# Kernel tuning notes

Hardware: AMD Instinct MI355X
Metric: run time of the kernel (lower is better)

Reference implementation:

```python
import jax, jax.numpy as jnp
import numpy as np

B, GS, IN, HID = 256, 32, 512, 1024
HW = GS * GS

def setup_inputs() -> dict:
    key = jax.random.key(0)
    ks = jax.random.split(key, 18)
    s = 0.02
    return {
        "grid": jax.random.normal(ks[0], (B, 1, GS, GS), jnp.float32),
        "conv1_w": jax.random.normal(ks[1], (8, 1, 3, 3), jnp.float32) * s,
        "conv1_b": jax.random.normal(ks[2], (8,), jnp.float32) * s,
        "conv2_w": jax.random.normal(ks[3], (16, 8, 3, 3), jnp.float32) * s,
        "conv2_b": jax.random.normal(ks[4], (16,), jnp.float32) * s,
        "lin_w": jax.random.normal(ks[5], (IN, HW * 16), jnp.float32) * s,
        "lin_b": jax.random.normal(ks[6], (IN,), jnp.float32) * s,
        "gru_wih": jax.random.normal(ks[7], (3 * HID, IN + HW + 1), jnp.float32) * s,
        "gru_whh": jax.random.normal(ks[8], (3 * HID, HID), jnp.float32) * s,
        "gru_bih": jax.random.normal(ks[9], (3 * HID,), jnp.float32) * s,
        "gru_bhh": jax.random.normal(ks[10], (3 * HID,), jnp.float32) * s,
        "write_w": jax.random.normal(ks[11], (HW, HID), jnp.float32) * s,
        "write_b": jax.random.normal(ks[12], (HW,), jnp.float32) * s,
        "inc_w": jax.random.normal(ks[13], (1, HID), jnp.float32) * s,
        "inc_b": jax.random.normal(ks[14], (1,), jnp.float32) * s,
        "term_w": jax.random.normal(ks[15], (1, HID), jnp.float32) * s,
        "term_b": jax.random.normal(ks[16], (1,), jnp.float32) * s,
        "max_steps": 100,
    }

def _conv(x, w, b):
    y = jax.lax.conv_general_dilated(x, w, (1, 1), "SAME",
                                     dimension_numbers=("NCHW", "OIHW", "NCHW"))
    return y + b[None, :, None, None]

def _gru_cell(x, h, wih, whh, bih, bhh):
    gi = x @ wih.T + bih            # (B, 3H)
    gh = h @ whh.T + bhh
    ir, iz, inn = jnp.split(gi, 3, axis=1)
    hr, hz, hn = jnp.split(gh, 3, axis=1)
    r = jax.nn.sigmoid(ir + hr)
    z = jax.nn.sigmoid(iz + hz)
    n = jnp.tanh(inn + r * hn)
    return (1.0 - z) * n + z * h

def reference(grid, conv1_w, conv1_b, conv2_w, conv2_b, lin_w, lin_b,
              gru_wih, gru_whh, gru_bih, gru_bhh,
              write_w, write_b, inc_w, inc_b, term_w, term_b, max_steps):
    bsz = grid.shape[0]
    feat = jax.nn.relu(_conv(grid, conv1_w, conv1_b))
    feat = jax.nn.relu(_conv(feat, conv2_w, conv2_b))
    feat = feat.reshape(bsz, -1) @ lin_w.T + lin_b     # (B, IN), torch Flatten is channel-major

    def step(carry, _):
        h, mask, count, done = carry
        x = jnp.concatenate([feat, mask, count], axis=1)
        h2 = _gru_cell(x, h, gru_wih, gru_whh, gru_bih, gru_bhh)
        write = jax.nn.sigmoid(h2 @ write_w.T + write_b)
        inc = jax.nn.sigmoid(h2 @ inc_w.T + inc_b)
        term = jax.nn.sigmoid(h2 @ term_w.T + term_b)
        upd = jnp.logical_not(done)
        h_n = jnp.where(upd, h2, h)
        mask_n = jnp.where(upd, mask + write, mask)
        count_n = jnp.where(upd, count + inc, count)
        done_n = jnp.logical_or(done, jnp.all(term > 0.5))
        return (h_n, mask_n, count_n, done_n), None

    init = (jnp.zeros((bsz, HID), grid.dtype),
            jnp.zeros((bsz, HW), grid.dtype),
            jnp.zeros((bsz, 1), grid.dtype),
            jnp.array(False))
    (h, mask, count, done), _ = jax.lax.scan(step, init, None, length=max_steps)
    return count, mask
```

## Files before the change

### kernel.cpp

```cpp
#include <hip/hip_runtime.h>
#include <hip/hip_cooperative_groups.h>

namespace cg = cooperative_groups;

#define DEVI static __device__ __forceinline__

typedef __attribute__((ext_vector_type(8))) short s8v;
typedef __attribute__((ext_vector_type(4))) float f32x4;
typedef unsigned short us_t;
typedef unsigned int u32;

constexpr int NT_ = 256;
constexpr int B_ = 256, HW_ = 1024, IN_ = 512, HID_ = 1024, H3_ = 3072;
constexpr int XD_ = 1537;
constexpr int FLAT_ = 16384;

constexpr int OFF_WIHFBF = 0;
constexpr int OFF_WIHM2  = 393216;
constexpr int OFF_WHHBF  = 3538944;
constexpr int OFF_WIHC   = 5111808;
constexpr int OFF_CNTD   = 5114880;
constexpr int OFF_FLAGS  = 5115136;
constexpr int OFF_FEATBF = 5115264;
constexpr int OFF_GI     = 5180800;
constexpr int OFF_GH     = 5967232;
constexpr int OFF_H0     = 6753664;
constexpr int OFF_H1     = 7015808;
constexpr int OFF_WSIG   = 7277952;
constexpr int OFF_HHI    = 7540096;
constexpr int OFF_WSIG2  = 7671168;
constexpr int OFF_C2BF   = 7933312;
constexpr int OFF_LINWBF = 10030464;
constexpr int OFF_PART = OFF_GI;
constexpr int OFF_PW   = OFF_C2BF;
constexpr int OFF_WWBF = 10292608;
constexpr int OFF_PA2  = 14224768;

struct Params {
  const float* grid;
  const float* c1w; const float* c1b;
  const float* c2w; const float* c2b;
  const float* linw; const float* linb;
  const float* wih; const float* whh;
  const float* bih; const float* bhh;
  const float* ww;  const float* wb;
  const float* incw; const float* incb;
  const float* termw; const float* termb;
  const int* max_steps;
  float* out;
  float* ws;
};

DEVI float sigm(float x) { return 1.f / (1.f + __expf(-x)); }
DEVI float tanh_(float x) { return 1.f - 2.f / (__expf(2.f * x) + 1.f); }
DEVI float2 ld2(const float* p) { return *(const float2*)p; }
DEVI void ld4(float* d, const float* p) {
  float4 v = *(const float4*)p; d[0] = v.x; d[1] = v.y; d[2] = v.z; d[3] = v.w;
}
DEVI us_t f2bf(float x) {
  union { float f; u32 u; } v; v.f = x;
  u32 r = v.u + 0x7FFFu + ((v.u >> 16) & 1u);
  return (us_t)(r >> 16);
}
DEVI float bf2f(us_t h) {
  union { u32 u; float f; } v; v.u = ((u32)h) << 16; return v.f;
}
DEVI u32 pack2(float a, float b) { return (u32)f2bf(a) | ((u32)f2bf(b) << 16); }

__global__ __launch_bounds__(NT_) void front_kernel(Params p) {
  __shared__ float smem[34 * 34 + 8 * 34 * 34];
  const int tid = threadIdx.x;
  if (blockIdx.x < 256) {
    float* s_in = smem;
    float* s_c1 = smem + 34 * 34;
    const int b = blockIdx.x;
    for (int i = tid; i < 34 * 34; i += NT_) s_in[i] = 0.f;
    for (int i = tid; i < 8 * 34 * 34; i += NT_) s_c1[i] = 0.f;
    __syncthreads();
    for (int i = tid; i < 1024; i += NT_) {
      int y = i >> 5, x = i & 31;
      s_in[(y + 1) * 34 + (x + 1)] = p.grid[b * 1024 + i];
    }
    __syncthreads();
    const int pos0 = tid * 4;
    const int y = pos0 >> 5, x0 = pos0 & 31;
    {
      float win[3][6];
      #pragma unroll
      for (int dy = 0; dy < 3; ++dy)
        #pragma unroll
        for (int c = 0; c < 6; ++c) win[dy][c] = s_in[(y + dy) * 34 + x0 + c];
      float acc[8][4];
      #pragma unroll
      for (int oc = 0; oc < 8; ++oc)
        #pragma unroll
        for (int i = 0; i < 4; ++i) acc[oc][i] = p.c1b[oc];
      #pragma unroll
      for (int oc = 0; oc < 8; ++oc)
        #pragma unroll
        for (int dy = 0; dy < 3; ++dy)
          #pragma unroll
          for (int dx = 0; dx < 3; ++dx) {
            float w = p.c1w[oc * 9 + dy * 3 + dx];
            #pragma unroll
            for (int i = 0; i < 4; ++i)
              acc[oc][i] = fmaf(w, win[dy][i + dx], acc[oc][i]);
          }
      #pragma unroll
      for (int oc = 0; oc < 8; ++oc)
        #pragma unroll
        for (int i = 0; i < 4; ++i)
          s_c1[oc * 1156 + (y + 1) * 34 + (x0 + i + 1)] = fmaxf(acc[oc][i], 0.f);
    }
    __syncthreads();
    {
      float acc[16][4];
      #pragma unroll
      for (int oc = 0; oc < 16; ++oc)
        #pragma unroll
        for (int i = 0; i < 4; ++i) acc[oc][i] = p.c2b[oc];
      for (int ic = 0; ic < 8; ++ic) {
        float win[3][6];
        #pragma unroll
        for (int dy = 0; dy < 3; ++dy)
          #pragma unroll
          for (int c = 0; c < 6; ++c)
            win[dy][c] = s_c1[ic * 1156 + (y + dy) * 34 + x0 + c];
        #pragma unroll
        for (int oc = 0; oc < 16; ++oc)
          #pragma unroll
          for (int dy = 0; dy < 3; ++dy)
            #pragma unroll
            for (int dx = 0; dx < 3; ++dx) {
              float w = p.c2w[oc * 72 + ic * 9 + dy * 3 + dx];
              #pragma unroll
              for (int i = 0; i < 4; ++i)
                acc[oc][i] = fmaf(w, win[dy][i + dx], acc[oc][i]);
            }
      }
      us_t* dst = (us_t*)(p.ws + OFF_C2BF) + b * FLAT_;
      #pragma unroll
      for (int oc = 0; oc < 16; ++oc) {
        u32 lo = pack2(fmaxf(acc[oc][0], 0.f), fmaxf(acc[oc][1], 0.f));
        u32 hi = pack2(fmaxf(acc[oc][2], 0.f), fmaxf(acc[oc][3], 0.f));
        *(uint2*)(dst + oc * 1024 + pos0) = make_uint2(lo, hi);
      }
    }
  } else {
    const int gt = (blockIdx.x - 256) * NT_ + tid;
    const int gs = 2048 * NT_;
    us_t* wihf = (us_t*)(p.ws + OFF_WIHFBF);
    us_t* wihm2 = (us_t*)(p.ws + OFF_WIHM2);
    us_t* whhbf = (us_t*)(p.ws + OFF_WHHBF);
    us_t* linwbf = (us_t*)(p.ws + OFF_LINWBF);
    float* wihc = p.ws + OFF_WIHC;
    int* flags = (int*)(p.ws + OFF_FLAGS);
    for (int i = gt; i < (IN_ * FLAT_) / 4; i += gs) {
      float4 v = *(const float4*)(p.linw + (size_t)i * 4);
      *(uint2*)(linwbf + (size_t)i * 4) = make_uint2(pack2(v.x, v.y), pack2(v.z, v.w));
    }
    for (int i = gt; i < (H3_ * HID_) / 4; i += gs) {
      float4 v = *(const float4*)(p.whh + (size_t)i * 4);
      *(uint2*)(whhbf + (size_t)i * 4) = make_uint2(pack2(v.x, v.y), pack2(v.z, v.w));
    }
    for (int i = gt; i < H3_ * IN_; i += gs) {
      int n = i >> 9, k = i & 511;
      wihf[i] = f2bf(p.wih[n * XD_ + k]);
    }
    for (int i = gt; i < H3_ * HID_; i += gs) {
      int n = i >> 10, k = i & 1023;
      float v = p.wih[n * XD_ + 512 + k];
      us_t hi = f2bf(v);
      wihm2[n * 2048 + k] = hi;
      wihm2[n * 2048 + 1024 + k] = f2bf(v - bf2f(hi));
    }
    for (int i = gt; i < H3_; i += gs) wihc[i] = p.wih[i * XD_ + 1536];
    for (int i = gt; i < 128; i += gs) flags[i] = 1;
  }
}

DEVI void mfma_block(const us_t* __restrict__ Ag, int lda,
                     const us_t* __restrict__ Bg, int ldb, int nc,
                     us_t* __restrict__ sA, us_t* __restrict__ sB,
                     float* __restrict__ dst, int ldd) {
  const int tid = threadIdx.x;
  const int ar = tid >> 3, au = tid & 7;
  const int sw = au ^ (ar & 7);
  const int abase = (ar * 8 + sw) * 8;
  const us_t* a0p = Ag + (size_t)ar * lda + au * 8;
  const us_t* a1p = Ag + (size_t)(ar + 32) * lda + au * 8;
  const us_t* b0p = Bg + (size_t)ar * ldb + au * 8;
  const us_t* b1p = b0p + (size_t)32 * ldb;
  const us_t* b2p = b0p + (size_t)64 * ldb;
  const us_t* b3p = b0p + (size_t)96 * ldb;
  f32x4 acc[4][2];
  #pragma unroll
  for (int f = 0; f < 4; ++f) { acc[f][0] = (f32x4)0.f; acc[f][1] = (f32x4)0.f; }
  s8v ra0 = *(const s8v*)a0p;
  s8v ra1 = *(const s8v*)a1p;
  s8v rb0 = *(const s8v*)b0p;
  s8v rb1 = *(const s8v*)b1p;
  s8v rb2 = *(const s8v*)b2p;
  s8v rb3 = *(const s8v*)b3p;
  const int w = tid >> 6;
  const int lane = tid & 63;
  const int l15 = lane & 15, l4 = lane >> 4;
  const int rsw = l15 & 7;
  int c = 0;
  for (;;) {
    __syncthreads();
    *(s8v*)(sA + abase) = ra0;
    *(s8v*)(sA + abase + 2048) = ra1;
    *(s8v*)(sB + abase) = rb0;
    *(s8v*)(sB + abase + 2048) = rb1;
    *(s8v*)(sB + abase + 4096) = rb2;
    *(s8v*)(sB + abase + 6144) = rb3;
    ++c;
    if (c < nc) {
      const int ko = c * 64;
      ra0 = *(const s8v*)(a0p + ko);
      ra1 = *(const s8v*)(a1p + ko);
      rb0 = *(const s8v*)(b0p + ko);
      rb1 = *(const s8v*)(b1p + ko);
      rb2 = *(const s8v*)(b2p + ko);
      rb3 = *(const s8v*)(b3p + ko);
    }
    __syncthreads();
    #pragma unroll
    for (int kk = 0; kk < 2; ++kk) {
      const int uoff = ((kk * 4 + l4) ^ rsw) * 8;
      s8v bA = *(const s8v*)(sB + (w * 32 + l15) * 64 + uoff);
      s8v bB = *(const s8v*)(sB + (w * 32 + 16 + l15) * 64 + uoff);
      #pragma unroll
      for (int f = 0; f < 4; ++f) {
        s8v a = *(const s8v*)(sA + (f * 16 + l15) * 64 + uoff);
        acc[f][0] = __builtin_amdgcn_mfma_f32_16x16x32_bf16(a, bA, acc[f][0], 0, 0, 0);
        acc[f][1] = __builtin_amdgcn_mfma_f32_16x16x32_bf16(a, bB, acc[f][1], 0, 0, 0);
      }
    }
    if (c >= nc) break;
  }
  #pragma unroll
  for (int f = 0; f < 4; ++f)
    #pragma unroll
    for (int g = 0; g < 2; ++g) {
      float* dp = dst + (size_t)(f * 16 + l4 * 4) * ldd + w * 32 + g * 16 + l15;
      #pragma unroll
      for (int j = 0; j < 4; ++j) dp[(size_t)j * ldd] = acc[f][g][j];
    }
}

__global__ __launch_bounds__(NT_) void lin_mfma(Params p) {
  __shared__ us_t sm[12288];
  const int b = blockIdx.x;
  const int ks = b & 15, t = b >> 4;
  const int mt = t >> 2, nt = t & 3;
  const us_t* A = (us_t*)(p.ws + OFF_C2BF) + (size_t)mt * 64 * FLAT_ + ks * 1024;
  const us_t* B = (us_t*)(p.ws + OFF_LINWBF) + (size_t)nt * 128 * FLAT_ + ks * 1024;
  float* dst = p.ws + OFF_PART + ks * (B_ * IN_) + mt * 64 * IN_ + nt * 128;
  mfma_block(A, FLAT_, B, FLAT_, 16, sm, sm + 4096, dst, IN_);
}

__global__ __launch_bounds__(NT_) void red_kernel(Params p) {
  const int gt = blockIdx.x * NT_ + threadIdx.x;
  {
    const int o = gt & (IN_ - 1);
    const float* part = p.ws + OFF_PART;
    float s = p.linb[o];
    #pragma unroll
    for (int ks = 0; ks < 16; ++ks) s += part[ks * (B_ * IN_) + gt];
    ((us_t*)(p.ws + OFF_FEATBF))[gt] = f2bf(s);
  }
  us_t* wwbf = (us_t*)(p.ws + OFF_WWBF);
  #pragma unroll
  for (int r = 0; r < 2; ++r) {
    const int j = gt + r * 131072;
    float4 v = *(const float4*)(p.ww + (size_t)j * 4);
    *(uint2*)(wwbf + (size_t)j * 4) = make_uint2(pack2(v.x, v.y), pack2(v.z, v.w));
  }
}

__global__ __launch_bounds__(NT_) void a1_mfma(Params p) {
  __shared__ us_t sm[12288];
  const int b = blockIdx.x;
  const int mt = b / 24, nt = b - mt * 24;
  const us_t* A = (us_t*)(p.ws + OFF_FEATBF) + (size_t)mt * 64 * IN_;
  const us_t* B = (us_t*)(p.ws + OFF_WIHFBF) + (size_t)nt * 128 * IN_;
  float* dst = p.ws + OFF_GI + (size_t)mt * 64 * H3_ + nt * 128;
  mfma_block(A, IN_, B, IN_, 8, sm, sm + 4096, dst, H3_);
}

__global__ __launch_bounds__(NT_) void stepA_mfma(Params p, int step) {
  if (((volatile int*)(p.ws + OFF_FLAGS))[step - 1]) return;
  __shared__ us_t sm[12288];
  const int b = blockIdx.x;
  if (b < 576) {
    const int term = b / 192;
    const int r = b - term * 192;
    const int ks = r / 96;
    const int t = r - ks * 96;
    const int mt = t / 24, nt = t - mt * 24;
    const us_t* A = (us_t*)(p.ws + OFF_WSIG2) + (size_t)mt * 64 * 2048 +
                    (term == 1 ? 1024 : 0) + ks * 512;
    const us_t* B = (us_t*)(p.ws + OFF_WIHM2) + (size_t)nt * 128 * 2048 +
                    (term == 2 ? 1024 : 0) + ks * 512;
    float* dst = p.ws + OFF_PA2 + (size_t)(term * 2 + ks) * 786432 +
                 (size_t)mt * 64 * H3_ + nt * 128;
    mfma_block(A, 2048, B, 2048, 8, sm, sm + 4096, dst, H3_);
  } else {
    const int r = b - 576;
    const int ks = r / 96;
    const int t = r - ks * 96;
    const int mt = t / 24, nt = t - mt * 24;
    const us_t* A = (us_t*)(p.ws + OFF_HHI) + (size_t)mt * 64 * HID_ + ks * 512;
    const us_t* B = (us_t*)(p.ws + OFF_WHHBF) + (size_t)nt * 128 * HID_ + ks * 512;
    float* dst = p.ws + OFF_PA2 + (size_t)(6 + ks) * 786432 +
                 (size_t)mt * 64 * H3_ + nt * 128;
    mfma_block(A, HID_, B, HID_, 8, sm, sm + 4096, dst, H3_);
  }
}

__global__ __launch_bounds__(NT_) void stepG_kernel(Params p, int step) {
  int* flags = (int*)(p.ws + OFF_FLAGS);
  if (step > 0 && ((volatile int*)flags)[step - 1]) return;
  __shared__ float sred[8];
  const int row = blockIdx.x;
  const int tid = threadIdx.x;
  const size_t base = (size_t)row * H3_;
  float* const gi = p.ws + OFF_GI + base;
  const float* const pA = p.ws + OFF_PA2;
  const float* const wihc = p.ws + OFF_WIHC;
  const float* hold = p.ws + ((step & 1) ? OFF_H1 : OFF_H0) + (size_t)row * HID_;
  float* hnew = p.ws + ((step & 1) ? OFF_H0 : OFF_H1) + (size_t)row * HID_;
  us_t* hhi = (us_t*)(p.ws + OFF_HHI) + (size_t)row * HID_;
  const float cd = (step > 0) ? (p.ws + OFF_CNTD)[row] : 0.f;
  float incd = 0.f, termd = 0.f;
  #pragma unroll
  for (int q = 0; q < 4; ++q) {
    const int c = tid + q * NT_;
    float gr_ = gi[c], gz_ = gi[1024 + c], gn_ = gi[2048 + c];
    float hr_ = 0.f, hz_ = 0.f, hn_ = 0.f, hv = 0.f;
    if (step > 0) {
      #pragma unroll
      for (int t6 = 0; t6 < 6; ++t6) {
        const float* pp = pA + (size_t)t6 * 786432 + base;
        gr_ += pp[c]; gz_ += pp[1024 + c]; gn_ += pp[2048 + c];
      }
      gr_ += cd * wihc[c];
      gz_ += cd * wihc[1024 + c];
      gn_ += cd * wihc[2048 + c];
      const float* q6 = pA + (size_t)6 * 786432 + base;
      const float* q7 = pA + (size_t)7 * 786432 + base;
      hr_ = q6[c] + q7[c];
      hz_ = q6[1024 + c] + q7[1024 + c];
      hn_ = q6[2048 + c] + q7[2048 + c];
      gi[c] = gr_; gi[1024 + c] = gz_; gi[2048 + c] = gn_;
      hv = hold[c];
    }
    float rr = sigm(gr_ + p.bih[c] + hr_ + p.bhh[c]);
    float zz = sigm(gz_ + p.bih[1024 + c] + hz_ + p.bhh[1024 + c]);
    float nn = tanh_(gn_ + p.bih[2048 + c] + rr * (hn_ + p.bhh[2048 + c]));
    float h2 = (1.f - zz) * nn + zz * hv;
    hnew[c] = h2;
    hhi[c] = f2bf(h2);
    incd = fmaf(h2, p.incw[c], incd);
    termd = fmaf(h2, p.termw[c], termd);
  }
  #pragma unroll
  for (int off = 32; off > 0; off >>= 1) {
    incd += __shfl_down(incd, off);
    termd += __shfl_down(termd, off);
  }
  if ((tid & 63) == 0) { sred[tid >> 6] = incd; sred[4 + (tid >> 6)] = termd; }
  __syncthreads();
  if (tid == 0) {
    float it = sred[0] + sred[1] + sred[2] + sred[3];
    float tt = sred[4] + sred[5] + sred[6] + sred[7];
    float cdn = sigm(it + p.incb[0]);
    (p.ws + OFF_CNTD)[row] = cdn;
    if (step == 0) p.out[row] = cdn;
    else p.out[row] += cdn;
    if (tt + p.termb[0] <= 0.f) atomicAnd(&flags[step], 0);
  }
}

__global__ __launch_bounds__(NT_) void stepW_mfma(Params p, int step) {
  if (step > 0 && ((volatile int*)(p.ws + OFF_FLAGS))[step - 1]) return;
  __shared__ us_t sm[12288];
  const int b = blockIdx.x;
  const int ks = b & 7, t = b >> 3;
  const int mt = t >> 3, nt = t & 7;
  const us_t* A = (us_t*)(p.ws + OFF_HHI) + (size_t)mt * 64 * HID_ + ks * 128;
  const us_t* B = (us_t*)(p.ws + OFF_WWBF) + (size_t)nt * 128 * HID_ + ks * 128;
  float* dst = p.ws + OFF_PW + ks * (B_ * HW_) + (size_t)mt * 64 * HW_ + nt * 128;
  mfma_block(A, HID_, B, HID_, 2, sm, sm + 4096, dst, HW_);
}

__global__ __launch_bounds__(NT_) void stepWepi_kernel(Params p, int step) {
  if (step > 0 && ((volatile int*)(p.ws + OFF_FLAGS))[step - 1]) return;
  const int i = (blockIdx.x * NT_ + threadIdx.x) * 4;
  const int m = i >> 10, n = i & 1023;
  const float* pW = p.ws + OFF_PW;
  float4 s = *(const float4*)(p.wb + n);
  #pragma unroll
  for (int ks = 0; ks < 8; ++ks) {
    float4 v = *(const float4*)(pW + ks * (B_ * HW_) + i);
    s.x += v.x; s.y += v.y; s.z += v.z; s.w += v.w;
  }
  float4 sv = {sigm(s.x), sigm(s.y), sigm(s.z), sigm(s.w)};
  float* op = p.out + B_ + i;
  if (step == 0) {
    *(float4*)op = sv;
  } else {
    float4 ov = *(float4*)op;
    ov.x += sv.x; ov.y += sv.y; ov.z += sv.z; ov.w += sv.w;
    *(float4*)op = ov;
  }
  *(float4*)(p.ws + OFF_WSIG + i) = sv;
  us_t* w2 = (us_t*)(p.ws + OFF_WSIG2) + (size_t)m * 2048 + n;
  us_t h0 = f2bf(sv.x), h1 = f2bf(sv.y), h2b = f2bf(sv.z), h3 = f2bf(sv.w);
  *(uint2*)w2 = make_uint2((u32)h0 | ((u32)h1 << 16), (u32)h2b | ((u32)h3 << 16));
  *(uint2*)(w2 + 1024) = make_uint2(
      pack2(sv.x - bf2f(h0), sv.y - bf2f(h1)),
      pack2(sv.z - bf2f(h2b), sv.w - bf2f(h3)));
}

DEVI void b_job(const Params& p, float* sh2, float* swb,
                const float* gi, const float* gh, const float* hold,
                float* hnew, float* wsig, float* cntd, int* dflag, int job) {
  const int tid = threadIdx.x;
  const int mt = job >> 3, nt = job & 7;
  const int r0 = mt * 8, c0 = nt * 128;
  const int gr = tid >> 5;
  const int gk = (tid & 31) * 2;
  const int wr = tid & 7;
  const int wc = (tid >> 3) * 4;
  const int row = r0 + gr;
  const float* giR = gi + row * H3_;
  const float* ghR = gh + row * H3_;
  const float* hR = hold + row * HID_;
  float* hW = hnew + row * HID_;
  float acc[4] = {0.f, 0.f, 0.f, 0.f};
  float incd = 0.f, termd = 0.f;
  const bool wh = (nt == 0);
  for (int kc = 0; kc < HID_; kc += 64) {
    float2 gxr = ld2(giR + kc + gk);
    float2 gxz = ld2(giR + 1024 + kc + gk);
    float2 gxn = ld2(giR + 2048 + kc + gk);
    float2 ghr = ld2(ghR + kc + gk);
    float2 ghz = ld2(ghR + 1024 + kc + gk);
    float2 ghn = ld2(ghR + 2048 + kc + gk);
    float2 hol = ld2(hR + kc + gk);
    float2 bri = ld2(p.bih + kc + gk);
    float2 brh = ld2(p.bhh + kc + gk);
    float2 bzi = ld2(p.bih + 1024 + kc + gk);
    float2 bzh = ld2(p.bhh + 1024 + kc + gk);
    float2 bni = ld2(p.bih + 2048 + kc + gk);
    float2 bnh = ld2(p.bhh + 2048 + kc + gk);
    float2 iw = ld2(p.incw + kc + gk);
    float2 tw = ld2(p.termw + kc + gk);
    float h2[2];
    {
      float rr = sigm(gxr.x + bri.x + ghr.x + brh.x);
      float zz = sigm(gxz.x + bzi.x + ghz.x + bzh.x);
      float nn = tanh_(gxn.x + bni.x + rr * (ghn.x + bnh.x));
      h2[0] = (1.f - zz) * nn + zz * hol.x;
      rr = sigm(gxr.y + bri.y + ghr.y + brh.y);
      zz = sigm(gxz.y + bzi.y + ghz.y + bzh.y);
      nn = tanh_(gxn.y + bni.y + rr * (ghn.y + bnh.y));
      h2[1] = (1.f - zz) * nn + zz * hol.y;
    }
    incd = fmaf(h2[0], iw.x, fmaf(h2[1], iw.y, incd));
    termd = fmaf(h2[0], tw.x, fmaf(h2[1], tw.y, termd));
    float4 wreg[8];
    #pragma unroll
    for (int it = 0; it < 8; ++it) {
      int id = tid + it * 256;
      int c = id >> 4, k4 = (id & 15) * 4;
      wreg[it] = *(const float4*)(p.ww + (c0 + c) * HID_ + kc + k4);
    }
    __syncthreads();
    sh2[gr * 68 + gk] = h2[0];
    sh2[gr * 68 + gk + 1] = h2[1];
    #pragma unroll
    for (int it = 0; it < 8; ++it) {
      int id = tid + it * 256;
      int c = id >> 4, k4 = (id & 15) * 4;
      swb[(k4 + 0) * 132 + c] = wreg[it].x;
      swb[(k4 + 1) * 132 + c] = wreg[it].y;
      swb[(k4 + 2) * 132 + c] = wreg[it].z;
      swb[(k4 + 3) * 132 + c] = wreg[it].w;
    }
    if (wh) {
      *(float2*)(hW + kc + gk) = make_float2(h2[0], h2[1]);
      *(u32*)((us_t*)(p.ws + OFF_HHI) + row * HID_ + kc + gk) = pack2(h2[0], h2[1]);
    }
    __syncthreads();
    #pragma unroll 8
    for (int kk = 0; kk < 64; ++kk) {
      float a = sh2[wr * 68 + kk];
      float4 b = *(const float4*)(swb + kk * 132 + wc);
      acc[0] = fmaf(a, b.x, acc[0]);
      acc[1] = fmaf(a, b.y, acc[1]);
      acc[2] = fmaf(a, b.z, acc[2]);
      acc[3] = fmaf(a, b.w, acc[3]);
    }
  }
  if (wh) {
    #pragma unroll
    for (int off = 16; off > 0; off >>= 1) {
      incd += __shfl_down(incd, off, 32);
      termd += __shfl_down(termd, off, 32);
    }
    if ((tid & 31) == 0) {
      float cd = sigm(incd + p.incb[0]);
      cntd[row] = cd;
      p.out[row] += cd;
      if (termd + p.termb[0] <= 0.f) atomicAnd(dflag, 0);
    }
  }
  {
    const int m = r0 + wr;
    float4 wb4 = *(const float4*)(p.wb + c0 + wc);
    float4 sv = {sigm(acc[0] + wb4.x), sigm(acc[1] + wb4.y),
                 sigm(acc[2] + wb4.z), sigm(acc[3] + wb4.w)};
    float* op = p.out + B_ + m * HW_ + c0 + wc;
    float4 ov = *(float4*)op;
    ov.x += sv.x; ov.y += sv.y; ov.z += sv.z; ov.w += sv.w;
    *(float4*)op = ov;
    *(float4*)(wsig + m * HID_ + c0 + wc) = sv;
    us_t* w2 = (us_t*)(p.ws + OFF_WSIG2) + m * 2048 + c0 + wc;
    us_t h0 = f2bf(sv.x), h1 = f2bf(sv.y), h2b = f2bf(sv.z), h3 = f2bf(sv.w);
    *(uint2*)w2 = make_uint2((u32)h0 | ((u32)h1 << 16), (u32)h2b | ((u32)h3 << 16));
    *(uint2*)(w2 + 1024) = make_uint2(
        pack2(sv.x - bf2f(h0), sv.y - bf2f(h1)),
        pack2(sv.z - bf2f(h2b), sv.w - bf2f(h3)));
  }
}

template <bool SB>
DEVI void gemm_db64(const float* __restrict__ A, int lda,
                    const float* __restrict__ Bw, int ldb, int K,
                    float* __restrict__ As, float* __restrict__ Bs,
                    float (&acc)[4][4]) {
  constexpr int P = 68;
  const int tid = threadIdx.x;
  const int tx = tid & 15, ty = tid >> 4;
  const int lr = tid >> 2, lk = (tid & 3) << 2;
  #pragma unroll
  for (int i = 0; i < 4; ++i)
    #pragma unroll
    for (int j = 0; j < 4; ++j) acc[i][j] = 0.f;
  auto ldb4 = [&](int k0) {
    float4 v;
    if constexpr (SB) {
      const float* q = Bw + (size_t)lr * ldb + k0 + lk;
      v.x = q[0]; v.y = q[1]; v.z = q[2]; v.w = q[3];
    } else {
      v = *(const float4*)(Bw + (size_t)lr * ldb + k0 + lk);
    }
    return v;
  };
  float4 va = *(const float4*)(A + lr * lda + lk);
  float4 vb = ldb4(0);
  As[(lk + 0) * P + lr] = va.x; As[(lk + 1) * P + lr] = va.y;
  As[(lk + 2) * P + lr] = va.z; As[(lk + 3) * P + lr] = va.w;
  Bs[(lk + 0) * P + lr] = vb.x; Bs[(lk + 1) * P + lr] = vb.y;
  Bs[(lk + 2) * P + lr] = vb.z; Bs[(lk + 3) * P + lr] = vb.w;
  __syncthreads();
  int cur = 0;
  for (int k0 = 16; k0 < K; k0 += 16) {
    va = *(const float4*)(A + lr * lda + k0 + lk);
    vb = ldb4(k0);
    const float* as = As + cur * (16 * P);
    const float* bs = Bs + cur * (16 * P);
    #pragma unroll
    for (int kk = 0; kk < 16; ++kk) {
      float a[4], b[4];
      ld4(a, as + kk * P + ty * 4);
      ld4(b, bs + kk * P + tx * 4);
      #pragma unroll
      for (int i = 0; i < 4; ++i)
        #pragma unroll
        for (int j = 0; j < 4; ++j) acc[i][j] = fmaf(a[i], b[j], acc[i][j]);
    }
    __syncthreads();
    float* asw = As + (cur ^ 1) * (16 * P);
    float* bsw = Bs + (cur ^ 1) * (16 * P);
    asw[(lk + 0) * P + lr] = va.x; asw[(lk + 1) * P + lr] = va.y;
    asw[(lk + 2) * P + lr] = va.z; asw[(lk + 3) * P + lr] = va.w;
    bsw[(lk + 0) * P + lr] = vb.x; bsw[(lk + 1) * P + lr] = vb.y;
    bsw[(lk + 2) * P + lr] = vb.z; bsw[(lk + 3) * P + lr] = vb.w;
    __syncthreads();
    cur ^= 1;
  }
  const float* as = As + cur * (16 * P);
  const float* bs = Bs + cur * (16 * P);
  #pragma unroll
  for (int kk = 0; kk < 16; ++kk) {
    float a[4], b[4];
    ld4(a, as + kk * P + ty * 4);
    ld4(b, bs + kk * P + tx * 4);
    #pragma unroll
    for (int i = 0; i < 4; ++i)
      #pragma unroll
      for (int j = 0; j < 4; ++j) acc[i][j] = fmaf(a[i], b[j], acc[i][j]);
  }
}

__global__ __launch_bounds__(NT_, 2) void tail_kernel(Params p, int start) {
  int* flags = (int*)(p.ws + OFF_FLAGS);
  if (((volatile int*)flags)[start - 1]) return;
  cg::grid_group gg = cg::this_grid();
  __shared__ __align__(16) float smem[8992];
  float* As = smem;
  float* Bs = smem + 2176;
  float* sh2 = smem;
  float* swb = smem + 544;
  float* const ws = p.ws;
  float* const gi = ws + OFF_GI;
  float* const gh = ws + OFF_GH;
  float* const wsig = ws + OFF_WSIG;
  float* const cntd = ws + OFF_CNTD;
  const float* const wihc = ws + OFF_WIHC;
  const int tid = threadIdx.x;
  const int bid = blockIdx.x;
  const int nb = gridDim.x;
  const int tx = tid & 15, ty = tid >> 4;
  const int msteps = p.max_steps[0];

  for (int step = start; step < msteps; ++step) {
    float* hcur = ws + ((step & 1) ? OFF_H1 : OFF_H0);
    float* hnxt = ws + ((step & 1) ? OFF_H0 : OFF_H1);
    for (int job = bid; job < 384; job += nb) {
      float acc[4][4];
      if (job < 192) {
        const int mt = job / 48, nt = job - mt * 48;
        gemm_db64<true>(wsig + mt * 64 * HID_, HID_,
                        p.wih + (size_t)nt * 64 * XD_ + 512, XD_, HID_, As, Bs, acc);
        #pragma unroll
        for (int i = 0; i < 4; ++i) {
          const int m = mt * 64 + ty * 4 + i;
          const float cd = cntd[m];
          float4 wc4 = *(const float4*)(wihc + nt * 64 + tx * 4);
          float* gp = gi + m * H3_ + nt * 64 + tx * 4;
          float4 g = *(float4*)gp;
          g.x += acc[i][0] + cd * wc4.x;
          g.y += acc[i][1] + cd * wc4.y;
          g.z += acc[i][2] + cd * wc4.z;
          g.w += acc[i][3] + cd * wc4.w;
          *(float4*)gp = g;
        }
      } else {
        const int j = job - 192;
        const int mt = j / 48, nt = j - mt * 48;
        gemm_db64<false>(hcur + mt * 64 * HID_, HID_,
                         p.whh + (size_t)nt * 64 * HID_, HID_, HID_, As, Bs, acc);
        #pragma unroll
        for (int i = 0; i < 4; ++i) {
          float4 v = {acc[i][0], acc[i][1], acc[i][2], acc[i][3]};
          *(float4*)(gh + (mt * 64 + ty * 4 + i) * H3_ + nt * 64 + tx * 4) = v;
        }
      }
      __syncthreads();
    }
    gg.sync();
    for (int job = bid; job < 256; job += nb)
      b_job(p, sh2, swb, gi, gh, hcur, hnxt, wsig, cntd, &flags[step], job);
    gg.sync();
    if (((volatile int*)flags)[step]) break;
  }
}

extern "C" void kernel_launch(void* const* d_in, const int* in_sizes, int n_in,
                              void* d_out, int out_size, void* d_ws, size_t ws_size,
                              hipStream_t stream) {
  (void)in_sizes; (void)n_in; (void)out_size; (void)ws_size;
  Params prm;
  prm.grid = (const float*)d_in[0];
  prm.c1w  = (const float*)d_in[1];
  prm.c1b  = (const float*)d_in[2];
  prm.c2w  = (const float*)d_in[3];
  prm.c2b  = (const float*)d_in[4];
  prm.linw = (const float*)d_in[5];
  prm.linb = (const float*)d_in[6];
  prm.wih  = (const float*)d_in[7];
  prm.whh  = (const float*)d_in[8];
  prm.bih  = (const float*)d_in[9];
  prm.bhh  = (const float*)d_in[10];
  prm.ww   = (const float*)d_in[11];
  prm.wb   = (const float*)d_in[12];
  prm.incw = (const float*)d_in[13];
  prm.incb = (const float*)d_in[14];
  prm.termw = (const float*)d_in[15];
  prm.termb = (const float*)d_in[16];
  prm.max_steps = (const int*)d_in[17];
  prm.out = (float*)d_out;
  prm.ws = (float*)d_ws;

  hipLaunchKernelGGL(front_kernel, dim3(2304), dim3(NT_), 0, stream, prm);
  hipLaunchKernelGGL(lin_mfma, dim3(256), dim3(NT_), 0, stream, prm);
  hipLaunchKernelGGL(red_kernel, dim3(512), dim3(NT_), 0, stream, prm);
  hipLaunchKernelGGL(a1_mfma, dim3(96), dim3(NT_), 0, stream, prm);

  constexpr int U = 2;
  hipLaunchKernelGGL(stepG_kernel, dim3(B_), dim3(NT_), 0, stream, prm, 0);
  hipLaunchKernelGGL(stepW_mfma, dim3(256), dim3(NT_), 0, stream, prm, 0);
  hipLaunchKernelGGL(stepWepi_kernel, dim3(256), dim3(NT_), 0, stream, prm, 0);
  for (int t = 1; t < U; ++t) {
    hipLaunchKernelGGL(stepA_mfma, dim3(768), dim3(NT_), 0, stream, prm, t);
    hipLaunchKernelGGL(stepG_kernel, dim3(B_), dim3(NT_), 0, stream, prm, t);
    hipLaunchKernelGGL(stepW_mfma, dim3(256), dim3(NT_), 0, stream, prm, t);
    hipLaunchKernelGGL(stepWepi_kernel, dim3(256), dim3(NT_), 0, stream, prm, t);
  }
  int start = U;
  void* args[] = {(void*)&prm, (void*)&start};
  (void)hipLaunchCooperativeKernel((const void*)tail_kernel, dim3(384), dim3(NT_),
                                   args, 0, stream);
}
```

Before: 138.8 us.

## Convert fp32 weights to bf16 on the fly inside MFMA loads

Drops the separate pre-conversion passes for lin_w, W_hh and write_w to bf16 scratch buffers. The MFMA tile loader now reads fp32 directly and packs to bf16 in registers. W_ih conversion moves into the feature-reduction kernel and reads W_ih rows contiguously. The lin_mfma block index is also permuted. This removes a large write-then-read of converted weights, at the cost of twice the global read bytes on the step kernels that reuse W_hh and write_w every timestep.

```diff
diff --git a/kernel.cpp b/kernel.cpp
--- a/kernel.cpp
+++ b/kernel.cpp
@@ -1,4 +1,5 @@
 #include <hip/hip_runtime.h>
+#include <hip/hip_bf16.h>
 #include <hip/hip_cooperative_groups.h>
 
 namespace cg = cooperative_groups;
@@ -17,7 +18,6 @@
 
 constexpr int OFF_WIHFBF = 0;
 constexpr int OFF_WIHM2  = 393216;
-constexpr int OFF_WHHBF  = 3538944;
 constexpr int OFF_WIHC   = 5111808;
 constexpr int OFF_CNTD   = 5114880;
 constexpr int OFF_FLAGS  = 5115136;
@@ -30,10 +30,8 @@
 constexpr int OFF_HHI    = 7540096;
 constexpr int OFF_WSIG2  = 7671168;
 constexpr int OFF_C2BF   = 7933312;
-constexpr int OFF_LINWBF = 10030464;
 constexpr int OFF_PART = OFF_GI;
 constexpr int OFF_PW   = OFF_C2BF;
-constexpr int OFF_WWBF = 10292608;
 constexpr int OFF_PA2  = 14224768;
 
 struct Params {
@@ -66,142 +64,124 @@
   union { u32 u; float f; } v; v.u = ((u32)h) << 16; return v.f;
 }
 DEVI u32 pack2(float a, float b) { return (u32)f2bf(a) | ((u32)f2bf(b) << 16); }
-
-__global__ __launch_bounds__(NT_) void front_kernel(Params p) {
-  __shared__ float smem[34 * 34 + 8 * 34 * 34];
+DEVI u32 pack2c(float a, float b) {
+  __hip_bfloat162 h = __float22bfloat162_rn(make_float2(a, b));
+  union { __hip_bfloat162 h; u32 u; } v; v.h = h; return v.u;
+}
+
+DEVI s8v ld8w(const us_t* p) { return *(const s8v*)p; }
+DEVI s8v ld8w(const float* p) {
+  float4 v0 = *(const float4*)p;
+  float4 v1 = *(const float4*)(p + 4);
+  union { u32 u[4]; s8v s; } r;
+  r.u[0] = pack2c(v0.x, v0.y); r.u[1] = pack2c(v0.z, v0.w);
+  r.u[2] = pack2c(v1.x, v1.y); r.u[3] = pack2c(v1.z, v1.w);
+  return r.s;
+}
+
+__global__ __launch_bounds__(NT_) void conv_kernel(Params p) {
+  __shared__ float s_in[34 * 34];
+  __shared__ float s_c1[8 * 34 * 34];
+  const int b = blockIdx.x;
   const int tid = threadIdx.x;
-  if (blockIdx.x < 256) {
-    float* s_in = smem;
-    float* s_c1 = smem + 34 * 34;
-    const int b = blockIdx.x;
-    for (int i = tid; i < 34 * 34; i += NT_) s_in[i] = 0.f;
-    for (int i = tid; i < 8 * 34 * 34; i += NT_) s_c1[i] = 0.f;
-    __syncthreads();
-    for (int i = tid; i < 1024; i += NT_) {
-      int y = i >> 5, x = i & 31;
-      s_in[(y + 1) * 34 + (x + 1)] = p.grid[b * 1024 + i];
-    }
-    __syncthreads();
-    const int pos0 = tid * 4;
-    const int y = pos0 >> 5, x0 = pos0 & 31;
-    {
-      float win[3][6];
+  for (int i = tid; i < 34 * 34; i += NT_) s_in[i] = 0.f;
+  for (int i = tid; i < 8 * 34 * 34; i += NT_) s_c1[i] = 0.f;
+  __syncthreads();
+  for (int i = tid; i < 1024; i += NT_) {
+    int y = i >> 5, x = i & 31;
+    s_in[(y + 1) * 34 + (x + 1)] = p.grid[b * 1024 + i];
+  }
+  __syncthreads();
+  const int pos0 = tid * 4;
+  const int y = pos0 >> 5, x0 = pos0 & 31;
+  {
+    float win[3][6];
+    #pragma unroll
+    for (int dy = 0; dy < 3; ++dy)
+      #pragma unroll
+      for (int c = 0; c < 6; ++c) win[dy][c] = s_in[(y + dy) * 34 + x0 + c];
+    float acc[8][4];
+    #pragma unroll
+    for (int oc = 0; oc < 8; ++oc)
+      #pragma unroll
+      for (int i = 0; i < 4; ++i) acc[oc][i] = p.c1b[oc];
+    #pragma unroll
+    for (int oc = 0; oc < 8; ++oc)
       #pragma unroll
       for (int dy = 0; dy < 3; ++dy)
         #pragma unroll
-        for (int c = 0; c < 6; ++c) win[dy][c] = s_in[(y + dy) * 34 + x0 + c];
-      float acc[8][4];
-      #pragma unroll
-      for (int oc = 0; oc < 8; ++oc)
+        for (int dx = 0; dx < 3; ++dx) {
+          float w = p.c1w[oc * 9 + dy * 3 + dx];
+          #pragma unroll
+          for (int i = 0; i < 4; ++i)
+            acc[oc][i] = fmaf(w, win[dy][i + dx], acc[oc][i]);
+        }
+    #pragma unroll
+    for (int oc = 0; oc < 8; ++oc)
+      #pragma unroll
+      for (int i = 0; i < 4; ++i)
+        s_c1[oc * 1156 + (y + 1) * 34 + (x0 + i + 1)] = fmaxf(acc[oc][i], 0.f);
+  }
+  __syncthreads();
+  {
+    float acc[16][4];
+    #pragma unroll
+    for (int oc = 0; oc < 16; ++oc)
+      #pragma unroll
+      for (int i = 0; i < 4; ++i) acc[oc][i] = p.c2b[oc];
+    for (int ic = 0; ic < 8; ++ic) {
+      float win[3][6];
+      #pragma unroll
+      for (int dy = 0; dy < 3; ++dy)
         #pragma unroll
-        for (int i = 0; i < 4; ++i) acc[oc][i] = p.c1b[oc];
-      #pragma unroll
-      for (int oc = 0; oc < 8; ++oc)
+        for (int c = 0; c < 6; ++c)
+          win[dy][c] = s_c1[ic * 1156 + (y + dy) * 34 + x0 + c];
+      #pragma unroll
+      for (int oc = 0; oc < 16; ++oc)
         #pragma unroll
         for (int dy = 0; dy < 3; ++dy)
           #pragma unroll
           for (int dx = 0; dx < 3; ++dx) {
-            float w = p.c1w[oc * 9 + dy * 3 + dx];
+            float w = p.c2w[oc * 72 + ic * 9 + dy * 3 + dx];
             #pragma unroll
             for (int i = 0; i < 4; ++i)
               acc[oc][i] = fmaf(w, win[dy][i + dx], acc[oc][i]);
           }
-      #pragma unroll
-      for (int oc = 0; oc < 8; ++oc)
-        #pragma unroll
-        for (int i = 0; i < 4; ++i)
-          s_c1[oc * 1156 + (y + 1) * 34 + (x0 + i + 1)] = fmaxf(acc[oc][i], 0.f);
-    }
-    __syncthreads();
-    {
-      float acc[16][4];
-      #pragma unroll
-      for (int oc = 0; oc < 16; ++oc)
-        #pragma unroll
-        for (int i = 0; i < 4; ++i) acc[oc][i] = p.c2b[oc];
-      for (int ic = 0; ic < 8; ++ic) {
-        float win[3][6];
-        #pragma unroll
-        for (int dy = 0; dy < 3; ++dy)
-          #pragma unroll
-          for (int c = 0; c < 6; ++c)
-            win[dy][c] = s_c1[ic * 1156 + (y + dy) * 34 + x0 + c];
-        #pragma unroll
-        for (int oc = 0; oc < 16; ++oc)
-          #pragma unroll
-          for (int dy = 0; dy < 3; ++dy)
-            #pragma unroll
-            for (int dx = 0; dx < 3; ++dx) {
-              float w = p.c2w[oc * 72 + ic * 9 + dy * 3 + dx];
-              #pragma unroll
-              for (int i = 0; i < 4; ++i)
-                acc[oc][i] = fmaf(w, win[dy][i + dx], acc[oc][i]);
-            }
-      }
-      us_t* dst = (us_t*)(p.ws + OFF_C2BF) + b * FLAT_;
-      #pragma unroll
-      for (int oc = 0; oc < 16; ++oc) {
-        u32 lo = pack2(fmaxf(acc[oc][0], 0.f), fmaxf(acc[oc][1], 0.f));
-        u32 hi = pack2(fmaxf(acc[oc][2], 0.f), fmaxf(acc[oc][3], 0.f));
-        *(uint2*)(dst + oc * 1024 + pos0) = make_uint2(lo, hi);
-      }
-    }
-  } else {
-    const int gt = (blockIdx.x - 256) * NT_ + tid;
-    const int gs = 2048 * NT_;
-    us_t* wihf = (us_t*)(p.ws + OFF_WIHFBF);
-    us_t* wihm2 = (us_t*)(p.ws + OFF_WIHM2);
-    us_t* whhbf = (us_t*)(p.ws + OFF_WHHBF);
-    us_t* linwbf = (us_t*)(p.ws + OFF_LINWBF);
-    float* wihc = p.ws + OFF_WIHC;
-    int* flags = (int*)(p.ws + OFF_FLAGS);
-    for (int i = gt; i < (IN_ * FLAT_) / 4; i += gs) {
-      float4 v = *(const float4*)(p.linw + (size_t)i * 4);
-      *(uint2*)(linwbf + (size_t)i * 4) = make_uint2(pack2(v.x, v.y), pack2(v.z, v.w));
-    }
-    for (int i = gt; i < (H3_ * HID_) / 4; i += gs) {
-      float4 v = *(const float4*)(p.whh + (size_t)i * 4);
-      *(uint2*)(whhbf + (size_t)i * 4) = make_uint2(pack2(v.x, v.y), pack2(v.z, v.w));
-    }
-    for (int i = gt; i < H3_ * IN_; i += gs) {
-      int n = i >> 9, k = i & 511;
-      wihf[i] = f2bf(p.wih[n * XD_ + k]);
-    }
-    for (int i = gt; i < H3_ * HID_; i += gs) {
-      int n = i >> 10, k = i & 1023;
-      float v = p.wih[n * XD_ + 512 + k];
-      us_t hi = f2bf(v);
-      wihm2[n * 2048 + k] = hi;
-      wihm2[n * 2048 + 1024 + k] = f2bf(v - bf2f(hi));
-    }
-    for (int i = gt; i < H3_; i += gs) wihc[i] = p.wih[i * XD_ + 1536];
-    for (int i = gt; i < 128; i += gs) flags[i] = 1;
-  }
-}
-
-DEVI void mfma_block(const us_t* __restrict__ Ag, int lda,
-                     const us_t* __restrict__ Bg, int ldb, int nc,
-                     us_t* __restrict__ sA, us_t* __restrict__ sB,
-                     float* __restrict__ dst, int ldd) {
+    }
+    us_t* dst = (us_t*)(p.ws + OFF_C2BF) + b * FLAT_;
+    #pragma unroll
+    for (int oc = 0; oc < 16; ++oc) {
+      u32 lo = pack2(fmaxf(acc[oc][0], 0.f), fmaxf(acc[oc][1], 0.f));
+      u32 hi = pack2(fmaxf(acc[oc][2], 0.f), fmaxf(acc[oc][3], 0.f));
+      *(uint2*)(dst + oc * 1024 + pos0) = make_uint2(lo, hi);
+    }
+  }
+}
+
+template <typename TA, typename TB>
+DEVI void mfma_blockT(const TA* __restrict__ Ag, int lda,
+                      const TB* __restrict__ Bg, int ldb, int nc,
+                      us_t* __restrict__ sA, us_t* __restrict__ sB,
+                      float* __restrict__ dst, int ldd) {
   const int tid = threadIdx.x;
   const int ar = tid >> 3, au = tid & 7;
   const int sw = au ^ (ar & 7);
   const int abase = (ar * 8 + sw) * 8;
-  const us_t* a0p = Ag + (size_t)ar * lda + au * 8;
-  const us_t* a1p = Ag + (size_t)(ar + 32) * lda + au * 8;
-  const us_t* b0p = Bg + (size_t)ar * ldb + au * 8;
-  const us_t* b1p = b0p + (size_t)32 * ldb;
-  const us_t* b2p = b0p + (size_t)64 * ldb;
-  const us_t* b3p = b0p + (size_t)96 * ldb;
+  const TA* a0p = Ag + (size_t)ar * lda + au * 8;
+  const TA* a1p = Ag + (size_t)(ar + 32) * lda + au * 8;
+  const TB* b0p = Bg + (size_t)ar * ldb + au * 8;
+  const TB* b1p = b0p + (size_t)32 * ldb;
+  const TB* b2p = b0p + (size_t)64 * ldb;
+  const TB* b3p = b0p + (size_t)96 * ldb;
   f32x4 acc[4][2];
   #pragma unroll
   for (int f = 0; f < 4; ++f) { acc[f][0] = (f32x4)0.f; acc[f][1] = (f32x4)0.f; }
-  s8v ra0 = *(const s8v*)a0p;
-  s8v ra1 = *(const s8v*)a1p;
-  s8v rb0 = *(const s8v*)b0p;
-  s8v rb1 = *(const s8v*)b1p;
-  s8v rb2 = *(const s8v*)b2p;
-  s8v rb3 = *(const s8v*)b3p;
+  s8v ra0 = ld8w(a0p);
+  s8v ra1 = ld8w(a1p);
+  s8v rb0 = ld8w(b0p);
+  s8v rb1 = ld8w(b1p);
+  s8v rb2 = ld8w(b2p);
+  s8v rb3 = ld8w(b3p);
   const int w = tid >> 6;
   const int lane = tid & 63;
   const int l15 = lane & 15, l4 = lane >> 4;
@@ -218,12 +198,12 @@
     ++c;
     if (c < nc) {
       const int ko = c * 64;
-      ra0 = *(const s8v*)(a0p + ko);
-      ra1 = *(const s8v*)(a1p + ko);
-      rb0 = *(const s8v*)(b0p + ko);
-      rb1 = *(const s8v*)(b1p + ko);
-      rb2 = *(const s8v*)(b2p + ko);
-      rb3 = *(const s8v*)(b3p + ko);
+      ra0 = ld8w(a0p + ko);
+      ra1 = ld8w(a1p + ko);
+      rb0 = ld8w(b0p + ko);
+      rb1 = ld8w(b1p + ko);
+      rb2 = ld8w(b2p + ko);
+      rb3 = ld8w(b3p + ko);
     }
     __syncthreads();
     #pragma unroll
@@ -252,31 +232,46 @@
 
 __global__ __launch_bounds__(NT_) void lin_mfma(Params p) {
   __shared__ us_t sm[12288];
-  const int b = blockIdx.x;
-  const int ks = b & 15, t = b >> 4;
-  const int mt = t >> 2, nt = t & 3;
+  const int j = (blockIdx.x >> 3) + (blockIdx.x & 7) * 32;
+  const int mt = j & 3, nt = (j >> 2) & 3, ks = j >> 4;
   const us_t* A = (us_t*)(p.ws + OFF_C2BF) + (size_t)mt * 64 * FLAT_ + ks * 1024;
-  const us_t* B = (us_t*)(p.ws + OFF_LINWBF) + (size_t)nt * 128 * FLAT_ + ks * 1024;
+  const float* B = p.linw + (size_t)nt * 128 * FLAT_ + ks * 1024;
   float* dst = p.ws + OFF_PART + ks * (B_ * IN_) + mt * 64 * IN_ + nt * 128;
-  mfma_block(A, FLAT_, B, FLAT_, 16, sm, sm + 4096, dst, IN_);
-}
-
-__global__ __launch_bounds__(NT_) void red_kernel(Params p) {
-  const int gt = blockIdx.x * NT_ + threadIdx.x;
-  {
+  mfma_blockT(A, FLAT_, B, FLAT_, 16, sm, sm + 4096, dst, IN_);
+}
+
+__global__ __launch_bounds__(NT_) void prepred_kernel(Params p) {
+  const int tid = threadIdx.x;
+  if (blockIdx.x < 512) {
+    const int gt = blockIdx.x * NT_ + tid;
     const int o = gt & (IN_ - 1);
     const float* part = p.ws + OFF_PART;
     float s = p.linb[o];
     #pragma unroll
     for (int ks = 0; ks < 16; ++ks) s += part[ks * (B_ * IN_) + gt];
     ((us_t*)(p.ws + OFF_FEATBF))[gt] = f2bf(s);
-  }
-  us_t* wwbf = (us_t*)(p.ws + OFF_WWBF);
-  #pragma unroll
-  for (int r = 0; r < 2; ++r) {
-    const int j = gt + r * 131072;
-    float4 v = *(const float4*)(p.ww + (size_t)j * 4);
-    *(uint2*)(wwbf + (size_t)j * 4) = make_uint2(pack2(v.x, v.y), pack2(v.z, v.w));
+  } else {
+    const int gt = (blockIdx.x - 512) * NT_ + tid;
+    const int gs = 1024 * NT_;
+    us_t* wihf = (us_t*)(p.ws + OFF_WIHFBF);
+    us_t* wihm2 = (us_t*)(p.ws + OFF_WIHM2);
+    float* wihc = p.ws + OFF_WIHC;
+    int* flags = (int*)(p.ws + OFF_FLAGS);
+    for (int i = gt; i < H3_ * XD_; i += gs) {
+      const int n = i / XD_, k = i - n * XD_;
+      const float v = p.wih[i];
+      if (k < 512) {
+        wihf[n * 512 + k] = f2bf(v);
+      } else if (k < 1536) {
+        const int kk = k - 512;
+        const us_t hi = f2bf(v);
+        wihm2[n * 2048 + kk] = hi;
+        wihm2[n * 2048 + 1024 + kk] = f2bf(v - bf2f(hi));
+      } else {
+        wihc[n] = v;
+      }
+    }
+    if (gt < 128) flags[gt] = 1;
   }
 }
 
@@ -287,7 +282,7 @@
   const us_t* A = (us_t*)(p.ws + OFF_FEATBF) + (size_t)mt * 64 * IN_;
   const us_t* B = (us_t*)(p.ws + OFF_WIHFBF) + (size_t)nt * 128 * IN_;
   float* dst = p.ws + OFF_GI + (size_t)mt * 64 * H3_ + nt * 128;
-  mfma_block(A, IN_, B, IN_, 8, sm, sm + 4096, dst, H3_);
+  mfma_blockT(A, IN_, B, IN_, 8, sm, sm + 4096, dst, H3_);
 }
 
 __global__ __launch_bounds__(NT_) void stepA_mfma(Params p, int step) {
@@ -306,17 +301,17 @@
                     (term == 2 ? 1024 : 0) + ks * 512;
     float* dst = p.ws + OFF_PA2 + (size_t)(term * 2 + ks) * 786432 +
                  (size_t)mt * 64 * H3_ + nt * 128;
-    mfma_block(A, 2048, B, 2048, 8, sm, sm + 4096, dst, H3_);
+    mfma_blockT(A, 2048, B, 2048, 8, sm, sm + 4096, dst, H3_);
   } else {
     const int r = b - 576;
     const int ks = r / 96;
     const int t = r - ks * 96;
     const int mt = t / 24, nt = t - mt * 24;
     const us_t* A = (us_t*)(p.ws + OFF_HHI) + (size_t)mt * 64 * HID_ + ks * 512;
-    const us_t* B = (us_t*)(p.ws + OFF_WHHBF) + (size_t)nt * 128 * HID_ + ks * 512;
+    const float* B = p.whh + (size_t)nt * 128 * HID_ + ks * 512;
     float* dst = p.ws + OFF_PA2 + (size_t)(6 + ks) * 786432 +
                  (size_t)mt * 64 * H3_ + nt * 128;
-    mfma_block(A, HID_, B, HID_, 8, sm, sm + 4096, dst, H3_);
+    mfma_blockT(A, HID_, B, HID_, 8, sm, sm + 4096, dst, H3_);
   }
 }
 
@@ -391,9 +386,9 @@
   const int ks = b & 7, t = b >> 3;
   const int mt = t >> 3, nt = t & 7;
   const us_t* A = (us_t*)(p.ws + OFF_HHI) + (size_t)mt * 64 * HID_ + ks * 128;
-  const us_t* B = (us_t*)(p.ws + OFF_WWBF) + (size_t)nt * 128 * HID_ + ks * 128;
+  const float* B = p.ww + (size_t)nt * 128 * HID_ + ks * 128;
   float* dst = p.ws + OFF_PW + ks * (B_ * HW_) + (size_t)mt * 64 * HW_ + nt * 128;
-  mfma_block(A, HID_, B, HID_, 2, sm, sm + 4096, dst, HW_);
+  mfma_blockT(A, HID_, B, HID_, 2, sm, sm + 4096, dst, HW_);
 }
 
 __global__ __launch_bounds__(NT_) void stepWepi_kernel(Params p, int step) {
@@ -698,9 +693,9 @@
   prm.out = (float*)d_out;
   prm.ws = (float*)d_ws;
 
-  hipLaunchKernelGGL(front_kernel, dim3(2304), dim3(NT_), 0, stream, prm);
+  hipLaunchKernelGGL(conv_kernel, dim3(B_), dim3(NT_), 0, stream, prm);
   hipLaunchKernelGGL(lin_mfma, dim3(256), dim3(NT_), 0, stream, prm);
-  hipLaunchKernelGGL(red_kernel, dim3(512), dim3(NT_), 0, stream, prm);
+  hipLaunchKernelGGL(prepred_kernel, dim3(1536), dim3(NT_), 0, stream, prm);
   hipLaunchKernelGGL(a1_mfma, dim3(96), dim3(NT_), 0, stream, prm);
 
   constexpr int U = 2;
```

New measurement: 142.8 us. +2.8%, slower.
